# Kernel tuning notes

Hardware: AMD Instinct MI355X
Metric: run time of the kernel (lower is better)

The kernel has to match this reference:

```python
import jax, jax.numpy as jnp
import numpy as np

N = 100_000      # nodes
E = 1_200_000    # edges (before self-loops)
F_IN = 128       # num_node_features
G = 256          # number of graphs in the batch
C = 10           # num_classes
NEG_SLOPE = 0.2  # PyG GATConv default


def setup_inputs() -> dict:
    key = jax.random.key(0)
    ks = jax.random.split(key, 20)
    x = jax.random.normal(ks[0], (N, F_IN), jnp.float32)
    edge_index = jax.random.randint(ks[1], (2, E), 0, N, dtype=jnp.int32)
    # sorted graph assignment covering all G graphs (no empty segments)
    batch = (jnp.arange(N, dtype=jnp.int32) * G) // N

    def lin(k, fi, fo):
        return jax.random.normal(k, (fi, fo), jnp.float32) * (1.0 / np.sqrt(fi))

    dims = [(F_IN, 16), (16, 32), (32, 64)]
    params = {}
    for i, (fi, fo) in enumerate(dims, start=1):
        params[f"W{i}"] = lin(ks[3 * i], fi, fo)
        params[f"a{i}_src"] = jax.random.normal(ks[3 * i + 1], (fo,), jnp.float32) * 0.1
        params[f"a{i}_dst"] = jax.random.normal(ks[3 * i + 2], (fo,), jnp.float32) * 0.1
        params[f"b{i}"] = jnp.zeros((fo,), jnp.float32)
    params["fc_w"] = lin(ks[15], 64, C)
    params["fc_b"] = jnp.zeros((C,), jnp.float32)
    return {"x": x, "edge_index": edge_index, "batch": batch, **params}


def _gat_layer(x, src, dst, W, a_src, a_dst, b):
    # h = Theta x; e_ij = LeakyReLU(a_src.h_j + a_dst.h_i), softmax over dst i
    h = x @ W                                     # [N, F]
    s = h @ a_src                                 # [N]
    d = h @ a_dst                                 # [N]
    logits = jax.nn.leaky_relu(s[src] + d[dst], NEG_SLOPE)   # [E+N]
    m = jax.ops.segment_max(logits, dst, num_segments=N)     # per-dst max
    ex = jnp.exp(logits - m[dst])
    denom = jax.ops.segment_sum(ex, dst, num_segments=N)
    alpha = ex / (denom[dst] + 1e-16)             # [E+N]
    out = jax.ops.segment_sum(alpha[:, None] * h[src], dst, num_segments=N)
    return out + b


def reference(x, edge_index, batch, W1, a1_src, a1_dst, b1, W2, a2_src, a2_dst, b2,
              W3, a3_src, a3_dst, b3, fc_w, fc_b):
    # add self-loops (PyG GATConv default) -> every dst segment non-empty
    loops = jnp.arange(N, dtype=edge_index.dtype)
    src = jnp.concatenate([edge_index[0], loops])
    dst = jnp.concatenate([edge_index[1], loops])

    h = jax.nn.relu(_gat_layer(x, src, dst, W1, a1_src, a1_dst, b1))
    # F.dropout(training=False) is a no-op in eval
    h = jax.nn.relu(_gat_layer(h, src, dst, W2, a2_src, a2_dst, b2))
    h = jax.nn.relu(_gat_layer(h, src, dst, W3, a3_src, a3_dst, b3))
    pooled = jax.ops.segment_max(h, batch, num_segments=G)   # global_max_pool [G, 64]
    logits = pooled @ fc_w + fc_b
    return jax.nn.log_softmax(logits, axis=1)
```

## Files before the change

### kernel.cpp

```cpp
#include <hip/hip_runtime.h>
#include <hip/hip_bf16.h>
#include <hip/hip_fp16.h>
#include <math.h>

#define NEG_SLOPE 0.2f
#define NCHUNK 1024
#define BSHIFT 9
#define BNODES 512

__device__ __forceinline__ float leaky(float x) { return x > 0.f ? x : NEG_SLOPE * x; }

__global__ void chunk_hist(const int* __restrict__ dst, int E, int Ec, int nbuck,
                           int* __restrict__ hmatT) {
    extern __shared__ int hist[];
    int c = blockIdx.x;
    for (int b = threadIdx.x; b < nbuck; b += 256) hist[b] = 0;
    __syncthreads();
    int lo = c * Ec, hi = min(E, lo + Ec);
    for (int e = lo + threadIdx.x; e < hi; e += 256) atomicAdd(&hist[dst[e] >> BSHIFT], 1);
    __syncthreads();
    for (int b = threadIdx.x; b < nbuck; b += 256) hmatT[b * NCHUNK + c] = hist[b];
}

__global__ void mat_scan(int* __restrict__ hmatT, int* __restrict__ btot) {
    __shared__ int wsum[4];
    int b = blockIdx.x;
    int t = threadIdx.x;
    int lane = t & 63, wave = t >> 6;
    int base = b * NCHUNK + t * 4;
    int a0 = hmatT[base], a1 = hmatT[base + 1], a2 = hmatT[base + 2], a3 = hmatT[base + 3];
    int ts = a0 + a1 + a2 + a3;
    int incl = ts;
#pragma unroll
    for (int o = 1; o < 64; o <<= 1) {
        int v = __shfl_up(incl, o);
        if (lane >= o) incl += v;
    }
    if (lane == 63) wsum[wave] = incl;
    __syncthreads();
    int wadd = 0;
#pragma unroll
    for (int w = 0; w < 4; w++) if (w < wave) wadd += wsum[w];
    int excl = wadd + incl - ts;
    hmatT[base] = excl;
    hmatT[base + 1] = excl + a0;
    hmatT[base + 2] = excl + a0 + a1;
    hmatT[base + 3] = excl + a0 + a1 + a2;
    if (t == 255) btot[b] = wadd + incl;
}

__global__ void base_scan(const int* __restrict__ btot, int nbuck, int* __restrict__ bbase,
                          int* __restrict__ offs, int N, int E) {
    __shared__ int tsum[256];
    int t = threadIdx.x;
    int v = (t < nbuck) ? btot[t] : 0;
    tsum[t] = v;
    __syncthreads();
    for (int o = 1; o < 256; o <<= 1) {
        int add = (t >= o) ? tsum[t - o] : 0;
        __syncthreads();
        tsum[t] += add;
        __syncthreads();
    }
    if (t <= nbuck) bbase[t] = (t == 0) ? 0 : tsum[t - 1];
    if (t == 0) offs[N] = N + E;
}

__global__ void chunk_scatter(const int* __restrict__ src, const int* __restrict__ dst,
                              int E, int Ec, int nbuck, const int* __restrict__ hmatT,
                              const int* __restrict__ bbase, int* __restrict__ bbuf) {
    extern __shared__ int cur[];
    int c = blockIdx.x;
    for (int b = threadIdx.x; b < nbuck; b += 256) cur[b] = bbase[b] + hmatT[b * NCHUNK + c];
    __syncthreads();
    int lo = c * Ec, hi = min(E, lo + Ec);
    for (int e = lo + threadIdx.x; e < hi; e += 256) {
        int d = dst[e];
        int b = d >> BSHIFT;
        int p = atomicAdd(&cur[b], 1);
        bbuf[p] = (src[e] << BSHIFT) | (d & (BNODES - 1));
    }
}

__global__ void bucket_build(const int* __restrict__ bbase, const int* __restrict__ bbuf,
                             int N, int* __restrict__ offs, int* __restrict__ csr) {
    __shared__ int hist[BNODES];
    __shared__ int offl[BNODES];
    __shared__ int cur[BNODES];
    int b = blockIdx.x;
    int t = threadIdx.x;
    hist[t] = 0;
    __syncthreads();
    int lo = bbase[b], hi = bbase[b + 1];
    for (int j = lo + t; j < hi; j += BNODES) atomicAdd(&hist[bbuf[j] & (BNODES - 1)], 1);
    __syncthreads();
    int own = hist[t];
    for (int o = 1; o < BNODES; o <<= 1) {
        int add = (t >= o) ? hist[t - o] : 0;
        __syncthreads();
        hist[t] += add;
        __syncthreads();
    }
    int excl = hist[t] - own;
    int n = (b << BSHIFT) + t;
    int off_n = n + bbase[b] + excl;
    offl[t] = off_n;
    cur[t] = 0;
    if (n < N) {
        offs[n] = off_n;
        csr[off_n] = n;
    }
    __syncthreads();
    for (int j = lo + t; j < hi; j += BNODES) {
        int v = bbuf[j];
        int ld = v & (BNODES - 1);
        int r = atomicAdd(&cur[ld], 1);
        csr[offl[ld] + 1 + r] = v >> BSHIFT;
    }
}


template <int FIN, int FOUT, typename Tin>
__global__ void transform(const Tin* __restrict__ xin, const float* __restrict__ W,
                          const float* __restrict__ asrc, const float* __restrict__ adst,
                          __half* __restrict__ h, float* __restrict__ sv, float* __restrict__ dv,
                          int N) {
    constexpr int TPN = FOUT / 4;
    constexpr int BN  = 256 / TPN;
    constexpr int PITCH = FIN + 4;
    __shared__ float xs[BN * PITCH];
    __shared__ float wl[FIN * FOUT];
    __shared__ float al[FOUT], bl[FOUT];
    for (int j = threadIdx.x; j < FIN * FOUT; j += 256) wl[j] = W[j];
    if (threadIdx.x < FOUT) { al[threadIdx.x] = asrc[threadIdx.x]; bl[threadIdx.x] = adst[threadIdx.x]; }
    int base = blockIdx.x * BN;
    constexpr int NV = BN * FIN / 4;
    int limv = ((N - base) * FIN) >> 2;
    for (int v = threadIdx.x; v < NV; v += 256) {
        int n = v / (FIN / 4), c = v % (FIN / 4);
        float4 val;
        if constexpr (sizeof(Tin) == 2) {
            const uint2* xg = (const uint2*)xin + (size_t)base * (FIN / 4);
            uint2 raw = (v < limv) ? xg[v] : make_uint2(0u, 0u);
            float2 f0 = __half22float2(*(const __half2*)&raw.x);
            float2 f1 = __half22float2(*(const __half2*)&raw.y);
            val = make_float4(f0.x, f0.y, f1.x, f1.y);
        } else {
            const float4* xg = (const float4*)xin + (size_t)base * (FIN / 4);
            val = (v < limv) ? xg[v] : make_float4(0.f, 0.f, 0.f, 0.f);
        }
        *(float4*)&xs[n * PITCH + c * 4] = val;
    }
    __syncthreads();
    int node_l = threadIdx.x / TPN;
    int fq = (threadIdx.x % TPN) * 4;
    int node = base + node_l;
    const float* xrow = &xs[node_l * PITCH];
    float4 acc = make_float4(0.f, 0.f, 0.f, 0.f);
#pragma unroll 8
    for (int k = 0; k < FIN; k++) {
        float xv = xrow[k];
        float4 w4 = *(const float4*)&wl[k * FOUT + fq];
        acc.x += xv * w4.x; acc.y += xv * w4.y; acc.z += xv * w4.z; acc.w += xv * w4.w;
    }
    if (node < N) {
        __half2* hp = (__half2*)(h + (size_t)node * FOUT + fq);
        hp[0] = __floats2half2_rn(acc.x, acc.y);
        hp[1] = __floats2half2_rn(acc.z, acc.w);
        float sp = acc.x * al[fq] + acc.y * al[fq + 1] + acc.z * al[fq + 2] + acc.w * al[fq + 3];
        float dp = acc.x * bl[fq] + acc.y * bl[fq + 1] + acc.z * bl[fq + 2] + acc.w * bl[fq + 3];
#pragma unroll
        for (int o = TPN / 2; o > 0; o >>= 1) { sp += __shfl_xor(sp, o); dp += __shfl_xor(dp, o); }
        if (fq == 0) { sv[node] = sp; dv[node] = dp; }
    }
}


template <int F>
__global__ void gat_fused(const __half* __restrict__ h, const float* __restrict__ sv,
                          const float* __restrict__ dv, const int* __restrict__ offs,
                          const int* __restrict__ csr, const float* __restrict__ bias,
                          __half* __restrict__ y, int N) {
    constexpr int L = F / 4;
    constexpr int NPB = 256 / L;
    int sub = threadIdx.x / L;
    int lane = threadIdx.x % L;
    int wlane = threadIdx.x & 63;
    int sgbase = wlane & ~(L - 1);
    int i = blockIdx.x * NPB + sub;
    if (i >= N) return;
    int beg = offs[i], end = offs[i + 1];
    float di = dv[i];
    float4 acc = make_float4(0.f, 0.f, 0.f, 0.f);
    float ssum = 0.f;
    int j = beg;
    for (; j + 4 <= end; j += 4) {
        int s0 = csr[j], s1 = csr[j + 1], s2 = csr[j + 2], s3 = csr[j + 3];
        uint2 u0 = *((const uint2*)(h + (size_t)s0 * F) + lane);
        uint2 u1 = *((const uint2*)(h + (size_t)s1 * F) + lane);
        uint2 u2 = *((const uint2*)(h + (size_t)s2 * F) + lane);
        uint2 u3 = *((const uint2*)(h + (size_t)s3 * F) + lane);
        int k = lane & 3;
        int sel = s0;
        if (k == 1) sel = s1; else if (k == 2) sel = s2; else if (k == 3) sel = s3;
        float myw = __expf(leaky(sv[sel] + di));
        float w0 = __shfl(myw, sgbase + 0);
        float w1 = __shfl(myw, sgbase + 1);
        float w2 = __shfl(myw, sgbase + 2);
        float w3 = __shfl(myw, sgbase + 3);
        ssum += (w0 + w1) + (w2 + w3);
        float2 a0 = __half22float2(*(const __half2*)&u0.x), c0 = __half22float2(*(const __half2*)&u0.y);
        float2 a1 = __half22float2(*(const __half2*)&u1.x), c1 = __half22float2(*(const __half2*)&u1.y);
        float2 a2 = __half22float2(*(const __half2*)&u2.x), c2 = __half22float2(*(const __half2*)&u2.y);
        float2 a3 = __half22float2(*(const __half2*)&u3.x), c3 = __half22float2(*(const __half2*)&u3.y);
        acc.x += w0 * a0.x + w1 * a1.x + w2 * a2.x + w3 * a3.x;
        acc.y += w0 * a0.y + w1 * a1.y + w2 * a2.y + w3 * a3.y;
        acc.z += w0 * c0.x + w1 * c1.x + w2 * c2.x + w3 * c3.x;
        acc.w += w0 * c0.y + w1 * c1.y + w2 * c2.y + w3 * c3.y;
    }
    for (; j < end; j++) {
        int srcj = csr[j];
        uint2 u = *((const uint2*)(h + (size_t)srcj * F) + lane);
        float w = __expf(leaky(sv[srcj] + di));
        ssum += w;
        float2 f0 = __half22float2(*(const __half2*)&u.x);
        float2 f1 = __half22float2(*(const __half2*)&u.y);
        acc.x += w * f0.x; acc.y += w * f0.y; acc.z += w * f1.x; acc.w += w * f1.y;
    }
    float inv = 1.0f / ssum;
    float4 b4 = ((const float4*)bias)[lane];
    float vx = fmaxf(acc.x * inv + b4.x, 0.f);
    float vy = fmaxf(acc.y * inv + b4.y, 0.f);
    float vz = fmaxf(acc.z * inv + b4.z, 0.f);
    float vw = fmaxf(acc.w * inv + b4.w, 0.f);
    __half2 o0 = __floats2half2_rn(vx, vy);
    __half2 o1 = __floats2half2_rn(vz, vw);
    uint2 st;
    st.x = *(unsigned int*)&o0;
    st.y = *(unsigned int*)&o1;
    ((uint2*)(y + (size_t)i * F))[lane] = st;
}


__global__ void pool_head(const __half* __restrict__ y, const float* __restrict__ fcw,
                          const float* __restrict__ fcb, float* __restrict__ out,
                          int N, int G, int C) {
    __shared__ float red[256];
    __shared__ float pl[64];
    int g = blockIdx.x;
    long long gl = g;
    int start = (int)((gl * N + G - 1) / G);
    int end = (int)(((gl + 1) * N + G - 1) / G);
    int f = threadIdx.x & 63, w = threadIdx.x >> 6;
    float m = 0.f;
    for (int i = start + w; i < end; i += 4) m = fmaxf(m, __half2float(y[(size_t)i * 64 + f]));
    red[threadIdx.x] = m;
    __syncthreads();
    if (threadIdx.x < 64) {
        pl[f] = fmaxf(fmaxf(red[f], red[64 + f]), fmaxf(red[128 + f], red[192 + f]));
    }
    __syncthreads();
    if (threadIdx.x < 64) {
        int c = threadIdx.x;
        float z = -1e30f;
        if (c < C) {
            z = fcb[c];
            for (int k = 0; k < 64; k++) z += pl[k] * fcw[k * 10 + c];
        }
        float zm = z;
#pragma unroll
        for (int o = 1; o < 16; o <<= 1) zm = fmaxf(zm, __shfl_xor(zm, o));
        float e = (c < C) ? __expf(z - zm) : 0.f;
        float se = e;
#pragma unroll
        for (int o = 1; o < 16; o <<= 1) se += __shfl_xor(se, o);
        if (c < C) out[g * C + c] = z - zm - logf(se);
    }
}


extern "C" void kernel_launch(void* const* d_in, const int* in_sizes, int n_in,
                              void* d_out, int out_size, void* d_ws, size_t ws_size,
                              hipStream_t stream) {
    const float* x    = (const float*)d_in[0];
    const int*   eidx = (const int*)d_in[1];
    const float* W1 = (const float*)d_in[3];
    const float* a1s = (const float*)d_in[4];
    const float* a1d = (const float*)d_in[5];
    const float* b1 = (const float*)d_in[6];
    const float* W2 = (const float*)d_in[7];
    const float* a2s = (const float*)d_in[8];
    const float* a2d = (const float*)d_in[9];
    const float* b2 = (const float*)d_in[10];
    const float* W3 = (const float*)d_in[11];
    const float* a3s = (const float*)d_in[12];
    const float* a3d = (const float*)d_in[13];
    const float* b3 = (const float*)d_in[14];
    const float* fcw = (const float*)d_in[15];
    const float* fcb = (const float*)d_in[16];
    float* out = (float*)d_out;

    const int N = in_sizes[2];
    const int E = in_sizes[1] / 2;
    const int C = in_sizes[16];
    const int G = out_size / C;

    const int* src = eidx;
    const int* dst = eidx + E;

    size_t off = 0;
    auto alloc = [&](size_t bytes) -> void* {
        void* p = (char*)d_ws + off;
        off += (bytes + 255) & ~(size_t)255;
        return p;
    };
    int* offs   = (int*)alloc((size_t)(N + 1) * 4);
    int* csr    = (int*)alloc((size_t)(E + N) * 4);
    float* sbuf = (float*)alloc((size_t)N * 4);
    float* dbuf = (float*)alloc((size_t)N * 4);
    __half* hbuf = (__half*)alloc((size_t)N * 64 * 2);
    __half* ybuf = (__half*)alloc((size_t)N * 64 * 2);

    const int NBUCK = (N + BNODES - 1) >> BSHIFT;
    const int Ec = (E + NCHUNK - 1) / NCHUNK;
    int* hmatT = (int*)alloc((size_t)NBUCK * NCHUNK * 4);
    int* btot  = (int*)alloc((size_t)NBUCK * 4);
    int* bbase = (int*)alloc((size_t)(NBUCK + 1) * 4);
    int* bbuf  = (int*)ybuf;

    const size_t histBytes = (size_t)NBUCK * 4;

    chunk_hist<<<NCHUNK, 256, histBytes, stream>>>(dst, E, Ec, NBUCK, hmatT);
    mat_scan<<<NBUCK, 256, 0, stream>>>(hmatT, btot);
    base_scan<<<1, 256, 0, stream>>>(btot, NBUCK, bbase, offs, N, E);
    chunk_scatter<<<NCHUNK, 256, histBytes, stream>>>(src, dst, E, Ec, NBUCK, hmatT, bbase, bbuf);
    bucket_build<<<NBUCK, BNODES, 0, stream>>>(bbase, bbuf, N, offs, csr);

    transform<128, 16, float><<<(N + 63) / 64, 256, 0, stream>>>(x, W1, a1s, a1d, hbuf, sbuf, dbuf, N);
    gat_fused<16><<<(N + 63) / 64, 256, 0, stream>>>(hbuf, sbuf, dbuf, offs, csr, b1, ybuf, N);
    transform<16, 32, __half><<<(N + 31) / 32, 256, 0, stream>>>(ybuf, W2, a2s, a2d, hbuf, sbuf, dbuf, N);
    gat_fused<32><<<(N + 31) / 32, 256, 0, stream>>>(hbuf, sbuf, dbuf, offs, csr, b2, ybuf, N);
    transform<32, 64, __half><<<(N + 15) / 16, 256, 0, stream>>>(ybuf, W3, a3s, a3d, hbuf, sbuf, dbuf, N);
    gat_fused<64><<<(N + 15) / 16, 256, 0, stream>>>(hbuf, sbuf, dbuf, offs, csr, b3, ybuf, N);

    pool_head<<<G, 256, 0, stream>>>(ybuf, fcw, fcb, out, N, G, C);
}
```

Measured before the change: 286.3 us.

## Fuse next-layer linear transform into GAT aggregation kernels

Adds a gat_trans kernel that, after softmax-weighted neighbour aggregation, applies bias+ReLU and immediately multiplies by the next layer's weight matrix, also computing the next layer's src/dst attention scores. This removes the intermediate activation write/read and two separate transform launches between layers. It uses ping-pong h/s/d buffers and costs extra shared memory for weights plus per-node shuffle work in the aggregation kernel.

```diff
diff --git a/kernel.cpp b/kernel.cpp
--- a/kernel.cpp
+++ b/kernel.cpp
@@ -120,8 +120,8 @@
 }
 
 
-template <int FIN, int FOUT, typename Tin>
-__global__ void transform(const Tin* __restrict__ xin, const float* __restrict__ W,
+template <int FIN, int FOUT>
+__global__ void transform(const float* __restrict__ xin, const float* __restrict__ W,
                           const float* __restrict__ asrc, const float* __restrict__ adst,
                           __half* __restrict__ h, float* __restrict__ sv, float* __restrict__ dv,
                           int N) {
@@ -135,20 +135,11 @@
     if (threadIdx.x < FOUT) { al[threadIdx.x] = asrc[threadIdx.x]; bl[threadIdx.x] = adst[threadIdx.x]; }
     int base = blockIdx.x * BN;
     constexpr int NV = BN * FIN / 4;
+    const float4* xg = (const float4*)xin + (size_t)base * (FIN / 4);
     int limv = ((N - base) * FIN) >> 2;
     for (int v = threadIdx.x; v < NV; v += 256) {
         int n = v / (FIN / 4), c = v % (FIN / 4);
-        float4 val;
-        if constexpr (sizeof(Tin) == 2) {
-            const uint2* xg = (const uint2*)xin + (size_t)base * (FIN / 4);
-            uint2 raw = (v < limv) ? xg[v] : make_uint2(0u, 0u);
-            float2 f0 = __half22float2(*(const __half2*)&raw.x);
-            float2 f1 = __half22float2(*(const __half2*)&raw.y);
-            val = make_float4(f0.x, f0.y, f1.x, f1.y);
-        } else {
-            const float4* xg = (const float4*)xin + (size_t)base * (FIN / 4);
-            val = (v < limv) ? xg[v] : make_float4(0.f, 0.f, 0.f, 0.f);
-        }
+        float4 val = (v < limv) ? xg[v] : make_float4(0.f, 0.f, 0.f, 0.f);
         *(float4*)&xs[n * PITCH + c * 4] = val;
     }
     __syncthreads();
@@ -173,6 +164,105 @@
         for (int o = TPN / 2; o > 0; o >>= 1) { sp += __shfl_xor(sp, o); dp += __shfl_xor(dp, o); }
         if (fq == 0) { sv[node] = sp; dv[node] = dp; }
     }
+}
+
+
+template <int FI, int FO>
+__global__ void gat_trans(const __half* __restrict__ h, const float* __restrict__ sv,
+                          const float* __restrict__ dv, const int* __restrict__ offs,
+                          const int* __restrict__ csr, const float* __restrict__ bias,
+                          const float* __restrict__ Wn, const float* __restrict__ an_s,
+                          const float* __restrict__ an_d,
+                          __half* __restrict__ h2, float* __restrict__ sv2,
+                          float* __restrict__ dv2, int N) {
+    constexpr int L = FI / 4;
+    constexpr int CPL = FO / L;
+    constexpr int NPB = 256 / L;
+    __shared__ float wl[FI * FO];
+    __shared__ float al[FO], bl[FO];
+    for (int j = threadIdx.x; j < FI * FO; j += 256) wl[j] = Wn[j];
+    if (threadIdx.x < FO) { al[threadIdx.x] = an_s[threadIdx.x]; bl[threadIdx.x] = an_d[threadIdx.x]; }
+    __syncthreads();
+    int sub = threadIdx.x / L;
+    int lane = threadIdx.x % L;
+    int wlane = threadIdx.x & 63;
+    int sgbase = wlane & ~(L - 1);
+    int i = blockIdx.x * NPB + sub;
+    if (i >= N) return;
+    int beg = offs[i], end = offs[i + 1];
+    float di = dv[i];
+    float4 acc = make_float4(0.f, 0.f, 0.f, 0.f);
+    float ssum = 0.f;
+    int j = beg;
+    for (; j + 4 <= end; j += 4) {
+        int s0 = csr[j], s1 = csr[j + 1], s2 = csr[j + 2], s3 = csr[j + 3];
+        uint2 u0 = *((const uint2*)(h + (size_t)s0 * FI) + lane);
+        uint2 u1 = *((const uint2*)(h + (size_t)s1 * FI) + lane);
+        uint2 u2 = *((const uint2*)(h + (size_t)s2 * FI) + lane);
+        uint2 u3 = *((const uint2*)(h + (size_t)s3 * FI) + lane);
+        int k = lane & 3;
+        int sel = s0;
+        if (k == 1) sel = s1; else if (k == 2) sel = s2; else if (k == 3) sel = s3;
+        float myw = __expf(leaky(sv[sel] + di));
+        float w0 = __shfl(myw, sgbase + 0);
+        float w1 = __shfl(myw, sgbase + 1);
+        float w2 = __shfl(myw, sgbase + 2);
+        float w3 = __shfl(myw, sgbase + 3);
+        ssum += (w0 + w1) + (w2 + w3);
+        float2 a0 = __half22float2(*(const __half2*)&u0.x), c0 = __half22float2(*(const __half2*)&u0.y);
+        float2 a1 = __half22float2(*(const __half2*)&u1.x), c1 = __half22float2(*(const __half2*)&u1.y);
+        float2 a2 = __half22float2(*(const __half2*)&u2.x), c2 = __half22float2(*(const __half2*)&u2.y);
+        float2 a3 = __half22float2(*(const __half2*)&u3.x), c3 = __half22float2(*(const __half2*)&u3.y);
+        acc.x += w0 * a0.x + w1 * a1.x + w2 * a2.x + w3 * a3.x;
+        acc.y += w0 * a0.y + w1 * a1.y + w2 * a2.y + w3 * a3.y;
+        acc.z += w0 * c0.x + w1 * c1.x + w2 * c2.x + w3 * c3.x;
+        acc.w += w0 * c0.y + w1 * c1.y + w2 * c2.y + w3 * c3.y;
+    }
+    for (; j < end; j++) {
+        int srcj = csr[j];
+        uint2 u = *((const uint2*)(h + (size_t)srcj * FI) + lane);
+        float w = __expf(leaky(sv[srcj] + di));
+        ssum += w;
+        float2 f0 = __half22float2(*(const __half2*)&u.x);
+        float2 f1 = __half22float2(*(const __half2*)&u.y);
+        acc.x += w * f0.x; acc.y += w * f0.y; acc.z += w * f1.x; acc.w += w * f1.y;
+    }
+    float inv = 1.0f / ssum;
+    float4 b4 = ((const float4*)bias)[lane];
+    float4 yv;
+    yv.x = fmaxf(acc.x * inv + b4.x, 0.f);
+    yv.y = fmaxf(acc.y * inv + b4.y, 0.f);
+    yv.z = fmaxf(acc.z * inv + b4.z, 0.f);
+    yv.w = fmaxf(acc.w * inv + b4.w, 0.f);
+    int colbase = lane * CPL;
+    float oacc[CPL];
+#pragma unroll
+    for (int c = 0; c < CPL; c++) oacc[c] = 0.f;
+#pragma unroll
+    for (int jj = 0; jj < L; jj++) {
+        float v0 = __shfl(yv.x, sgbase + jj);
+        float v1 = __shfl(yv.y, sgbase + jj);
+        float v2 = __shfl(yv.z, sgbase + jj);
+        float v3 = __shfl(yv.w, sgbase + jj);
+        const float* w0 = &wl[(jj * 4 + 0) * FO + colbase];
+        const float* w1 = &wl[(jj * 4 + 1) * FO + colbase];
+        const float* w2 = &wl[(jj * 4 + 2) * FO + colbase];
+        const float* w3 = &wl[(jj * 4 + 3) * FO + colbase];
+#pragma unroll
+        for (int c = 0; c < CPL; c++)
+            oacc[c] += v0 * w0[c] + v1 * w1[c] + v2 * w2[c] + v3 * w3[c];
+    }
+    __half2 hp[CPL / 2];
+#pragma unroll
+    for (int c = 0; c < CPL / 2; c++) hp[c] = __floats2half2_rn(oacc[2 * c], oacc[2 * c + 1]);
+    *((uint2*)(h2 + (size_t)i * FO + colbase)) = *(uint2*)&hp[0];
+    *((uint2*)(h2 + (size_t)i * FO + colbase + 4)) = *(uint2*)&hp[2];
+    float sp = 0.f, dp = 0.f;
+#pragma unroll
+    for (int c = 0; c < CPL; c++) { sp += oacc[c] * al[colbase + c]; dp += oacc[c] * bl[colbase + c]; }
+#pragma unroll
+    for (int o = 1; o < L; o <<= 1) { sp += __shfl_xor(sp, o); dp += __shfl_xor(dp, o); }
+    if (lane == 0) { sv2[i] = sp; dv2[i] = dp; }
 }
 
 
@@ -316,17 +406,19 @@
     };
     int* offs   = (int*)alloc((size_t)(N + 1) * 4);
     int* csr    = (int*)alloc((size_t)(E + N) * 4);
-    float* sbuf = (float*)alloc((size_t)N * 4);
-    float* dbuf = (float*)alloc((size_t)N * 4);
-    __half* hbuf = (__half*)alloc((size_t)N * 64 * 2);
-    __half* ybuf = (__half*)alloc((size_t)N * 64 * 2);
+    float* sbufA = (float*)alloc((size_t)N * 4);
+    float* dbufA = (float*)alloc((size_t)N * 4);
+    float* sbufB = (float*)alloc((size_t)N * 4);
+    float* dbufB = (float*)alloc((size_t)N * 4);
+    __half* hA = (__half*)alloc((size_t)N * 64 * 2);
+    __half* hB = (__half*)alloc((size_t)N * 64 * 2);
 
     const int NBUCK = (N + BNODES - 1) >> BSHIFT;
     const int Ec = (E + NCHUNK - 1) / NCHUNK;
     int* hmatT = (int*)alloc((size_t)NBUCK * NCHUNK * 4);
     int* btot  = (int*)alloc((size_t)NBUCK * 4);
     int* bbase = (int*)alloc((size_t)(NBUCK + 1) * 4);
-    int* bbuf  = (int*)ybuf;
+    int* bbuf  = (int*)hB;
 
     const size_t histBytes = (size_t)NBUCK * 4;
 
@@ -336,12 +428,12 @@
     chunk_scatter<<<NCHUNK, 256, histBytes, stream>>>(src, dst, E, Ec, NBUCK, hmatT, bbase, bbuf);
     bucket_build<<<NBUCK, BNODES, 0, stream>>>(bbase, bbuf, N, offs, csr);
 
-    transform<128, 16, float><<<(N + 63) / 64, 256, 0, stream>>>(x, W1, a1s, a1d, hbuf, sbuf, dbuf, N);
-    gat_fused<16><<<(N + 63) / 64, 256, 0, stream>>>(hbuf, sbuf, dbuf, offs, csr, b1, ybuf, N);
-    transform<16, 32, __half><<<(N + 31) / 32, 256, 0, stream>>>(ybuf, W2, a2s, a2d, hbuf, sbuf, dbuf, N);
-    gat_fused<32><<<(N + 31) / 32, 256, 0, stream>>>(hbuf, sbuf, dbuf, offs, csr, b2, ybuf, N);
-    transform<32, 64, __half><<<(N + 15) / 16, 256, 0, stream>>>(ybuf, W3, a3s, a3d, hbuf, sbuf, dbuf, N);
-    gat_fused<64><<<(N + 15) / 16, 256, 0, stream>>>(hbuf, sbuf, dbuf, offs, csr, b3, ybuf, N);
-
-    pool_head<<<G, 256, 0, stream>>>(ybuf, fcw, fcb, out, N, G, C);
-}
+    transform<128, 16><<<(N + 63) / 64, 256, 0, stream>>>(x, W1, a1s, a1d, hA, sbufA, dbufA, N);
+    gat_trans<16, 32><<<(N + 63) / 64, 256, 0, stream>>>(hA, sbufA, dbufA, offs, csr, b1,
+                                                         W2, a2s, a2d, hB, sbufB, dbufB, N);
+    gat_trans<32, 64><<<(N + 31) / 32, 256, 0, stream>>>(hB, sbufB, dbufB, offs, csr, b2,
+                                                         W3, a3s, a3d, hA, sbufA, dbufA, N);
+    gat_fused<64><<<(N + 15) / 16, 256, 0, stream>>>(hA, sbufA, dbufA, offs, csr, b3, hB, N);
+
+    pool_head<<<G, 256, 0, stream>>>(hB, fcw, fcb, out, N, G, C);
+}
```

New measurement: 279.4 us. 2.4% less time.
